# Optimization experiments

Measured on AMD Instinct MI355X. Metric: run time of the kernel, lower is better.

Reference implementation:

```python
import jax, jax.numpy as jnp
import numpy as np

KEYS = 11     # inference_keys: number of heatmap channels / keypoints
NSTACK = 4
B, H, W = 16, 128, 128


def setup_inputs() -> dict:
    key = jax.random.key(0)
    k1, k2, k3 = jax.random.split(key, 3)
    combined_preds = jax.random.normal(k1, (B, NSTACK, 2 * KEYS, H, W), dtype=jnp.float32)
    heatmaps = jax.random.uniform(k2, (B, KEYS, H, W), dtype=jnp.float32)
    # labels[..., 9] and [..., 10] are keypoint coords; scale to [0, 160) so some
    # fall outside [0, H)=[0,128) and exercise the validity-mask branch.
    labels = jax.random.uniform(k3, (B, KEYS, 11), dtype=jnp.float32) * 160.0
    return {"combined_preds": combined_preds, "heatmaps": heatmaps, "labels": labels}


def reference(combined_preds, heatmaps, labels):
    keys = KEYS
    hm = combined_preds[:, :, :keys]          # [B, S, K, H, W] heatmap preds
    lb = combined_preds[:, :, keys:]          # [B, S, K, H, W] label preds
    b, s, k, m, n = hm.shape                  # m = H, n = W (code uses m for both // and %)

    # HeatmapLoss per stack, vectorized over the stack dim
    heat_loss = ((hm - heatmaps[:, None]) ** 2).sum(axis=(2, 3, 4))  # [B, S]

    # LabelLoss, fully vectorized over (B, S, K)
    flat = hm.reshape(b, s, k, m * n)
    index = jnp.argmax(flat, axis=-1)         # [B, S, K]
    x = index // m                            # matches int(index / m) in original
    y = index % m
    # a[x, y] where a is the [H, W] heatmap -> flat[x * W + y]
    a_xy = jnp.take_along_axis(flat, (x * n + y)[..., None], axis=-1)[..., 0]

    pred = lb.reshape(b, s, k, -1)            # [B, S, K, H*W]
    lab = labels[:, None]                     # [B, 1, K, 11] broadcast over stacks

    gx, gy = lab[..., 9], lab[..., 10]
    valid = (gx > 0) & (gy > 0) & (gx < m) & (gy < n)

    xf = x.astype(pred.dtype)
    yf = y.astype(pred.dtype)
    xy_loss = (gx + lab[..., 7] - xf - pred[..., 7]) ** 2 \
            + (gy + lab[..., 8] - yf - pred[..., 8]) ** 2
    conf_loss = (1.0 - a_xy) ** 2
    class_loss = ((pred[..., 0:7] - lab[..., 0:7]) ** 2).sum(axis=-1)

    per_kp = jnp.where(valid, class_loss + xy_loss + conf_loss, 0.0)  # [B, S, K]
    label_loss = per_kp.sum(axis=-1)                                   # [B, S]

    return heat_loss, label_loss
```

## Files before the change

kernel.cpp:

```cpp
#include <hip/hip_runtime.h>
#include <math.h>

#define KEYS 11
#define NSTACK 4
#define NB 16
#define HH 128
#define WW 128
#define HW (HH * WW)

typedef float f4 __attribute__((ext_vector_type(4)));

__global__ __launch_bounds__(256) void kp_main(
    const float* __restrict__ cp,
    const float* __restrict__ heat,
    const float* __restrict__ lab,
    float* __restrict__ ws)
{
    const int grp = blockIdx.x;
    const int b = grp / KEYS;
    const int k = grp % KEYS;
    const int tid = threadIdx.x;

    const f4* __restrict__ ht4 = (const f4*)(heat + (size_t)grp * HW);
    const f4* __restrict__ hm0 = (const f4*)(cp + ((size_t)((b * NSTACK + 0) * (2 * KEYS) + k)) * HW);
    const f4* __restrict__ hm1 = (const f4*)(cp + ((size_t)((b * NSTACK + 1) * (2 * KEYS) + k)) * HW);
    const f4* __restrict__ hm2 = (const f4*)(cp + ((size_t)((b * NSTACK + 2) * (2 * KEYS) + k)) * HW);
    const f4* __restrict__ hm3 = (const f4*)(cp + ((size_t)((b * NSTACK + 3) * (2 * KEYS) + k)) * HW);

    float sum[NSTACK]  = {0.0f, 0.0f, 0.0f, 0.0f};
    float vmax[NSTACK] = {-INFINITY, -INFINITY, -INFINITY, -INFINITY};
    int   imax[NSTACK] = {0, 0, 0, 0};

    #pragma unroll 4
    for (int i = tid; i < HW / 4; i += 256) {
        f4 c = __builtin_nontemporal_load(ht4 + i);
        f4 a[NSTACK];
        a[0] = __builtin_nontemporal_load(hm0 + i);
        a[1] = __builtin_nontemporal_load(hm1 + i);
        a[2] = __builtin_nontemporal_load(hm2 + i);
        a[3] = __builtin_nontemporal_load(hm3 + i);
        const int base = i * 4;
        #pragma unroll
        for (int s = 0; s < NSTACK; ++s) {
            float d0 = a[s][0] - c[0], d1 = a[s][1] - c[1];
            float d2 = a[s][2] - c[2], d3 = a[s][3] - c[3];
            sum[s] += d0 * d0 + d1 * d1 + d2 * d2 + d3 * d3;
            if (a[s][0] > vmax[s]) { vmax[s] = a[s][0]; imax[s] = base;     }
            if (a[s][1] > vmax[s]) { vmax[s] = a[s][1]; imax[s] = base + 1; }
            if (a[s][2] > vmax[s]) { vmax[s] = a[s][2]; imax[s] = base + 2; }
            if (a[s][3] > vmax[s]) { vmax[s] = a[s][3]; imax[s] = base + 3; }
        }
    }

    #pragma unroll
    for (int off = 32; off > 0; off >>= 1) {
        #pragma unroll
        for (int s = 0; s < NSTACK; ++s) {
            float ov = __shfl_down(vmax[s], off);
            int   oi = __shfl_down(imax[s], off);
            float os = __shfl_down(sum[s],  off);
            sum[s] += os;
            if (ov > vmax[s] || (ov == vmax[s] && oi < imax[s])) { vmax[s] = ov; imax[s] = oi; }
        }
    }

    __shared__ float s_sum[4][NSTACK];
    __shared__ float s_v[4][NSTACK];
    __shared__ int   s_i[4][NSTACK];
    const int wave = tid >> 6;
    if ((tid & 63) == 0) {
        #pragma unroll
        for (int s = 0; s < NSTACK; ++s) {
            s_sum[wave][s] = sum[s]; s_v[wave][s] = vmax[s]; s_i[wave][s] = imax[s];
        }
    }
    __syncthreads();

    if (tid < NSTACK) {
        const int s = tid;
        float fsum = s_sum[0][s];
        float fv   = s_v[0][s];
        int   fi   = s_i[0][s];
        #pragma unroll
        for (int w = 1; w < 4; w++) {
            fsum += s_sum[w][s];
            if (s_v[w][s] > fv || (s_v[w][s] == fv && s_i[w][s] < fi)) {
                fv = s_v[w][s]; fi = s_i[w][s];
            }
        }
        ws[grp * NSTACK + s] = fsum;

        const float* __restrict__ lb = cp + ((size_t)((b * NSTACK + s) * (2 * KEYS) + KEYS + k)) * HW;
        const float* __restrict__ L  = lab + (size_t)grp * 11;
        float gx = L[9], gy = L[10];
        bool valid = (gx > 0.0f) && (gy > 0.0f) && (gx < (float)HH) && (gy < (float)WW);
        float loss = 0.0f;
        if (valid) {
            float xf = (float)(fi / WW);
            float yf = (float)(fi % WW);
            float dx = gx + L[7] - xf - lb[7];
            float dy = gy + L[8] - yf - lb[8];
            loss = dx * dx + dy * dy;
            float cm = 1.0f - fv;
            loss += cm * cm;
            #pragma unroll
            for (int j = 0; j < 7; j++) {
                float d = lb[j] - L[j];
                loss += d * d;
            }
        }
        ws[NB * KEYS * NSTACK + grp * NSTACK + s] = loss;
    }
}

__global__ void kp_final(const float* __restrict__ ws, float* __restrict__ out) {
    const int bs = threadIdx.x;
    const int b = bs / NSTACK;
    const int s = bs % NSTACK;
    float h = 0.0f, l = 0.0f;
    #pragma unroll
    for (int k = 0; k < KEYS; ++k) {
        const int g = b * KEYS + k;
        h += ws[g * NSTACK + s];
        l += ws[NB * KEYS * NSTACK + g * NSTACK + s];
    }
    out[bs] = h;
    out[64 + bs] = l;
}

extern "C" void kernel_launch(void* const* d_in, const int* in_sizes, int n_in,
                              void* d_out, int out_size, void* d_ws, size_t ws_size,
                              hipStream_t stream) {
    const float* cp   = (const float*)d_in[0];
    const float* heat = (const float*)d_in[1];
    const float* lab  = (const float*)d_in[2];
    float* out = (float*)d_out;
    float* ws  = (float*)d_ws;

    kp_main<<<NB * KEYS, 256, 0, stream>>>(cp, heat, lab, ws);
    kp_final<<<1, 64, 0, stream>>>(ws, out);
}
```

Before: 143.9 us.

## Split each keypoint's spatial reduction into four chunks across blocks

The main kernel now launches four blocks per (batch, keypoint) group instead of one. Each block reduces a quarter of the heatmap and writes partial sums, maxima and argmax indices to workspace. The final kernel merges the partials, computes the label loss and reduces per batch and stack. The goal is to fill more compute units than the previous 176 blocks on a bandwidth-bound kernel, at the cost of a slightly heavier serial final kernel.

```diff
diff --git a/kernel.cpp b/kernel.cpp
--- a/kernel.cpp
+++ b/kernel.cpp
@@ -7,43 +7,52 @@
 #define HH 128
 #define WW 128
 #define HW (HH * WW)
+#define NGRP (NB * KEYS)
+#define NCHUNK 4
+#define CF4 (HW / 4 / NCHUNK)
 
 typedef float f4 __attribute__((ext_vector_type(4)));
+
+#define WS_SUM 0
+#define WS_V   (NGRP * NCHUNK * NSTACK)
+#define WS_I   (2 * NGRP * NCHUNK * NSTACK)
 
 __global__ __launch_bounds__(256) void kp_main(
     const float* __restrict__ cp,
     const float* __restrict__ heat,
-    const float* __restrict__ lab,
     float* __restrict__ ws)
 {
-    const int grp = blockIdx.x;
+    const int bid = blockIdx.x;
+    const int c   = bid & (NCHUNK - 1);
+    const int grp = bid >> 2;
     const int b = grp / KEYS;
     const int k = grp % KEYS;
     const int tid = threadIdx.x;
 
-    const f4* __restrict__ ht4 = (const f4*)(heat + (size_t)grp * HW);
-    const f4* __restrict__ hm0 = (const f4*)(cp + ((size_t)((b * NSTACK + 0) * (2 * KEYS) + k)) * HW);
-    const f4* __restrict__ hm1 = (const f4*)(cp + ((size_t)((b * NSTACK + 1) * (2 * KEYS) + k)) * HW);
-    const f4* __restrict__ hm2 = (const f4*)(cp + ((size_t)((b * NSTACK + 2) * (2 * KEYS) + k)) * HW);
-    const f4* __restrict__ hm3 = (const f4*)(cp + ((size_t)((b * NSTACK + 3) * (2 * KEYS) + k)) * HW);
+    const int coff = c * CF4;
+    const f4* __restrict__ ht4 = (const f4*)(heat + (size_t)grp * HW) + coff;
+    const f4* __restrict__ hm0 = (const f4*)(cp + ((size_t)((b * NSTACK + 0) * (2 * KEYS) + k)) * HW) + coff;
+    const f4* __restrict__ hm1 = (const f4*)(cp + ((size_t)((b * NSTACK + 1) * (2 * KEYS) + k)) * HW) + coff;
+    const f4* __restrict__ hm2 = (const f4*)(cp + ((size_t)((b * NSTACK + 2) * (2 * KEYS) + k)) * HW) + coff;
+    const f4* __restrict__ hm3 = (const f4*)(cp + ((size_t)((b * NSTACK + 3) * (2 * KEYS) + k)) * HW) + coff;
 
     float sum[NSTACK]  = {0.0f, 0.0f, 0.0f, 0.0f};
     float vmax[NSTACK] = {-INFINITY, -INFINITY, -INFINITY, -INFINITY};
     int   imax[NSTACK] = {0, 0, 0, 0};
 
-    #pragma unroll 4
-    for (int i = tid; i < HW / 4; i += 256) {
-        f4 c = __builtin_nontemporal_load(ht4 + i);
+    #pragma unroll
+    for (int i = tid; i < CF4; i += 256) {
+        f4 cv = __builtin_nontemporal_load(ht4 + i);
         f4 a[NSTACK];
         a[0] = __builtin_nontemporal_load(hm0 + i);
         a[1] = __builtin_nontemporal_load(hm1 + i);
         a[2] = __builtin_nontemporal_load(hm2 + i);
         a[3] = __builtin_nontemporal_load(hm3 + i);
-        const int base = i * 4;
+        const int base = (coff + i) * 4;
         #pragma unroll
         for (int s = 0; s < NSTACK; ++s) {
-            float d0 = a[s][0] - c[0], d1 = a[s][1] - c[1];
-            float d2 = a[s][2] - c[2], d3 = a[s][3] - c[3];
+            float d0 = a[s][0] - cv[0], d1 = a[s][1] - cv[1];
+            float d2 = a[s][2] - cv[2], d3 = a[s][3] - cv[3];
             sum[s] += d0 * d0 + d1 * d1 + d2 * d2 + d3 * d3;
             if (a[s][0] > vmax[s]) { vmax[s] = a[s][0]; imax[s] = base;     }
             if (a[s][1] > vmax[s]) { vmax[s] = a[s][1]; imax[s] = base + 1; }
@@ -88,10 +97,45 @@
                 fv = s_v[w][s]; fi = s_i[w][s];
             }
         }
-        ws[grp * NSTACK + s] = fsum;
+        const int idx = (grp * NCHUNK + c) * NSTACK + s;
+        ws[WS_SUM + idx] = fsum;
+        ws[WS_V   + idx] = fv;
+        ws[WS_I   + idx] = __int_as_float(fi);
+    }
+}
+
+__global__ __launch_bounds__(768) void kp_final(
+    const float* __restrict__ cp,
+    const float* __restrict__ lab,
+    const float* __restrict__ ws,
+    float* __restrict__ out)
+{
+    __shared__ float sh[NGRP * NSTACK];
+    __shared__ float sl[NGRP * NSTACK];
+    const int t = threadIdx.x;
+
+    if (t < NGRP * NSTACK) {
+        const int g = t >> 2;
+        const int s = t & 3;
+        const int b = g / KEYS;
+        const int k = g % KEYS;
+
+        float fsum = 0.0f;
+        float fv   = -INFINITY;
+        int   fi   = 0;
+        #pragma unroll
+        for (int c = 0; c < NCHUNK; ++c) {
+            const int idx = (g * NCHUNK + c) * NSTACK + s;
+            float ps = ws[WS_SUM + idx];
+            float pv = ws[WS_V   + idx];
+            int   pi = __float_as_int(ws[WS_I + idx]);
+            fsum += ps;
+            if (pv > fv || (pv == fv && pi < fi)) { fv = pv; fi = pi; }
+        }
+        sh[t] = fsum;
 
         const float* __restrict__ lb = cp + ((size_t)((b * NSTACK + s) * (2 * KEYS) + KEYS + k)) * HW;
-        const float* __restrict__ L  = lab + (size_t)grp * 11;
+        const float* __restrict__ L  = lab + (size_t)g * 11;
         float gx = L[9], gy = L[10];
         bool valid = (gx > 0.0f) && (gy > 0.0f) && (gx < (float)HH) && (gy < (float)WW);
         float loss = 0.0f;
@@ -109,23 +153,23 @@
                 loss += d * d;
             }
         }
-        ws[NB * KEYS * NSTACK + grp * NSTACK + s] = loss;
+        sl[t] = loss;
     }
-}
+    __syncthreads();
 
-__global__ void kp_final(const float* __restrict__ ws, float* __restrict__ out) {
-    const int bs = threadIdx.x;
-    const int b = bs / NSTACK;
-    const int s = bs % NSTACK;
-    float h = 0.0f, l = 0.0f;
-    #pragma unroll
-    for (int k = 0; k < KEYS; ++k) {
-        const int g = b * KEYS + k;
-        h += ws[g * NSTACK + s];
-        l += ws[NB * KEYS * NSTACK + g * NSTACK + s];
+    if (t < NB * NSTACK) {
+        const int b = t / NSTACK;
+        const int s = t % NSTACK;
+        float h = 0.0f, l = 0.0f;
+        #pragma unroll
+        for (int k = 0; k < KEYS; ++k) {
+            const int g = b * KEYS + k;
+            h += sh[g * NSTACK + s];
+            l += sl[g * NSTACK + s];
+        }
+        out[t] = h;
+        out[64 + t] = l;
     }
-    out[bs] = h;
-    out[64 + bs] = l;
 }
 
 extern "C" void kernel_launch(void* const* d_in, const int* in_sizes, int n_in,
@@ -137,6 +181,6 @@
     float* out = (float*)d_out;
     float* ws  = (float*)d_ws;
 
-    kp_main<<<NB * KEYS, 256, 0, stream>>>(cp, heat, lab, ws);
-    kp_final<<<1, 64, 0, stream>>>(ws, out);
+    kp_main<<<NGRP * NCHUNK, 256, 0, stream>>>(cp, heat, ws);
+    kp_final<<<1, 768, 0, stream>>>(cp, lab, ws, out);
 }
```

Result: faster. 134.0 us (-6.8%).
